# Performance work log

Hardware: AMD Instinct MI355X
Metric: run time of the kernel (lower is better)

## Reference

```python
import jax, jax.numpy as jnp
import numpy as np

B, MBITS, P = 4096, 64, 64
BLK = P // 8          # 8: block size for crop-robust pattern
FREQ = P // 4         # 16: low-res frequency pattern size
KS, SIGMA = 5, 1.0


def _interp_matrix(n_in, n_out):
    # 1D bilinear interpolation matrix with align_corners=True semantics
    pos = jnp.arange(n_out, dtype=jnp.float32) * (n_in - 1) / (n_out - 1)
    lo = jnp.floor(pos).astype(jnp.int32)
    hi = jnp.minimum(lo + 1, n_in - 1)
    w = pos - lo.astype(jnp.float32)
    rows = jnp.arange(n_out)
    M = jnp.zeros((n_out, n_in), jnp.float32)
    M = M.at[rows, lo].add(1.0 - w).at[rows, hi].add(w)
    return M


def _gaussian_kernel(ks, sigma):
    c = jnp.arange(ks, dtype=jnp.float32) - ks // 2
    g = jnp.exp(-c**2 / (2.0 * sigma**2))
    g = g / g.sum()
    k2 = jnp.outer(g, g)
    return k2 / k2.sum()


def setup_inputs() -> dict:
    key = jax.random.key(0)
    ks = jax.random.split(key, 8)

    def lin(k, fan_in, fan_out):
        lim = 1.0 / np.sqrt(fan_in)
        return jax.random.uniform(k, (fan_in, fan_out), jnp.float32, -lim, lim)

    return {
        'message': jax.random.uniform(ks[0], (B, MBITS), jnp.float32),
        'sW1': lin(ks[1], MBITS, 256), 'sb1': jnp.zeros((256,), jnp.float32),
        'sW2': lin(ks[2], 256, 512),   'sb2': jnp.zeros((512,), jnp.float32),
        'sW3': lin(ks[3], 512, P * P), 'sb3': jnp.zeros((P * P,), jnp.float32),
        'fW1': lin(ks[4], MBITS, 128), 'fb1': jnp.zeros((128,), jnp.float32),
        'fW2': lin(ks[5], 128, FREQ * FREQ), 'fb2': jnp.zeros((FREQ * FREQ,), jnp.float32),
    }


def reference(message, sW1, sb1, sW2, sb2, sW3, sb3, fW1, fb1, fW2, fb2):
    b = message.shape[0]
    # --- spatial pattern: MLP -> tanh -> [B,1,P,P]
    h = jax.nn.relu(message @ sW1 + sb1)
    h = jax.nn.relu(h @ sW2 + sb2)
    spatial = jnp.tanh(h @ sW3 + sb3).reshape(b, 1, P, P)

    # --- frequency pattern: MLP -> tanh -> [B,1,16,16] -> bilinear upsample to PxP
    f = jax.nn.relu(message @ fW1 + fb1)
    freq_lo = jnp.tanh(f @ fW2 + fb2).reshape(b, FREQ, FREQ)
    M = _interp_matrix(FREQ, P)  # [P, FREQ]
    freq = jnp.einsum('ph,bhw,qw->bpq', M, freq_lo, M)[:, None]  # [B,1,P,P]

    # --- block pattern: bit i -> 8x8 block (row-major over an 8x8 grid)
    blocks = message.reshape(b, 8, 8)  # [B, rows, cols] of bits
    block = jnp.repeat(jnp.repeat(blocks, BLK, axis=1), BLK, axis=2)[:, None]  # [B,1,P,P]

    rgb = jnp.concatenate([spatial, freq, block], axis=1)  # [B,3,P,P]

    # --- depthwise 5x5 Gaussian smoothing, groups=3
    k2 = _gaussian_kernel(KS, SIGMA)
    kernel = jnp.broadcast_to(k2, (3, 1, KS, KS))
    out = jax.lax.conv_general_dilated(
        rgb, kernel, window_strides=(1, 1), padding=[(KS // 2, KS // 2)] * 2,
        dimension_numbers=('NCHW', 'OIHW', 'NCHW'), feature_group_count=3)
    return out
```

## Files before the change

kernel.cpp:

```cpp
#include <hip/hip_runtime.h>
#include <math.h>

#define BATCH 4096

typedef __attribute__((ext_vector_type(8))) short short8;
typedef __attribute__((ext_vector_type(4))) float f32x4;

__device__ __forceinline__ unsigned short f2bf(float f) {
  unsigned int u = __float_as_uint(f);
  u += 0x7FFF + ((u >> 16) & 1);
  return (unsigned short)(u >> 16);
}

__device__ __forceinline__ float bf2f(unsigned short s) {
  return __uint_as_float(((unsigned int)s) << 16);
}

__device__ __forceinline__ float fast_tanh(float x) {
  const float e = __expf(2.0f * x);
  const float r = __builtin_amdgcn_rcpf(e + 1.0f);
  return fmaf(-2.0f, r, 1.0f);
}

#define GLL16(g, l)                                                    \
  __builtin_amdgcn_global_load_lds(                                    \
      (const __attribute__((address_space(1))) unsigned int*)(g),      \
      (__attribute__((address_space(3))) unsigned int*)(l), 16, 0, 0)

__global__ __launch_bounds__(256) void prep_kernel(
    const float* __restrict__ sW1, const float* __restrict__ sW2,
    const float* __restrict__ sW3, const float* __restrict__ msg,
    unsigned short* __restrict__ w1T, unsigned short* __restrict__ w2T,
    unsigned short* __restrict__ w3T, unsigned short* __restrict__ msgb) {
  const int b = blockIdx.x;
  const int t = threadIdx.x;

  if (b >= 2192) {
    const int i0 = (b - 2192) * 2048 + t * 8;
    const float4 v0 = *reinterpret_cast<const float4*>(&msg[i0]);
    const float4 v1 = *reinterpret_cast<const float4*>(&msg[i0 + 4]);
    short8 o;
    o[0] = (short)f2bf(v0.x); o[1] = (short)f2bf(v0.y);
    o[2] = (short)f2bf(v0.z); o[3] = (short)f2bf(v0.w);
    o[4] = (short)f2bf(v1.x); o[5] = (short)f2bf(v1.y);
    o[6] = (short)f2bf(v1.z); o[7] = (short)f2bf(v1.w);
    *reinterpret_cast<short8*>(&msgb[i0]) = o;
    return;
  }

  const float* src;
  unsigned short* dst;
  int K, N, lgtN, tile;
  if (b < 16) {
    src = sW1; dst = w1T; K = 64; N = 256; lgtN = 3; tile = b;
  } else if (b < 144) {
    src = sW2; dst = w2T; K = 256; N = 512; lgtN = 4; tile = b - 16;
  } else {
    src = sW3; dst = w3T; K = 512; N = 4096; lgtN = 7; tile = b - 144;
  }
  const int ty = tile >> lgtN;
  const int tx = tile & ((1 << lgtN) - 1);

  __shared__ float tl[32][33];
  {
    const int r = t >> 3, c4 = (t & 7) * 4;
    const float4 v =
        *reinterpret_cast<const float4*>(&src[(size_t)(ty * 32 + r) * N + tx * 32 + c4]);
    tl[r][c4 + 0] = v.x; tl[r][c4 + 1] = v.y;
    tl[r][c4 + 2] = v.z; tl[r][c4 + 3] = v.w;
  }
  __syncthreads();
  {
    const int nl = t >> 3, k4 = (t & 7) * 4;
    unsigned short o[4];
#pragma unroll
    for (int i = 0; i < 4; ++i) o[i] = f2bf(tl[k4 + i][nl]);
    *reinterpret_cast<ushort4*>(&dst[(size_t)(tx * 32 + nl) * K + ty * 32 + k4]) =
        *reinterpret_cast<const ushort4*>(o);
  }
}

template <int ACT, int OBF16, int KDIM>
__global__ __launch_bounds__(256) void gemm_mfma(
    const unsigned short* __restrict__ A, const unsigned short* __restrict__ BT,
    const float* __restrict__ bias, void* __restrict__ Cv, int ldc) {
  __shared__ __align__(16) unsigned short As[128 * 32];
  __shared__ __align__(16) unsigned short Bs[128 * 32];

  const int t = threadIdx.x;
  const int lane = t & 63;
  const int w = t >> 6;
  const int bm = blockIdx.x * 128;
  const int bn = blockIdx.y * 128;

  const int r0 = w * 32 + (lane >> 2);
  const int r1 = r0 + 16;
  const int c0 = (lane & 3) ^ ((r0 >> 1) & 3);
  const int c1 = (lane & 3) ^ ((r1 >> 1) & 3);

  const unsigned short* gA0 = A + (size_t)(bm + r0) * KDIM + c0 * 8;
  const unsigned short* gA1 = A + (size_t)(bm + r1) * KDIM + c1 * 8;
  const unsigned short* gB0 = BT + (size_t)(bn + r0) * KDIM + c0 * 8;
  const unsigned short* gB1 = BT + (size_t)(bn + r1) * KDIM + c1 * 8;

  unsigned short* lA0 = &As[(w * 2 + 0) * 512];
  unsigned short* lA1 = &As[(w * 2 + 1) * 512];
  unsigned short* lB0 = &Bs[(w * 2 + 0) * 512];
  unsigned short* lB1 = &Bs[(w * 2 + 1) * 512];

  const int wm = (w >> 1) * 64;
  const int wn = (w & 1) * 64;
  const int lr = lane & 15;
  const int lc = lane >> 4;
  int aoff[4], boff[4];
#pragma unroll
  for (int i = 0; i < 4; ++i) {
    const int row = wm + i * 16 + lr;
    aoff[i] = row * 32 + (lc ^ ((row >> 1) & 3)) * 8;
    const int col = wn + i * 16 + lr;
    boff[i] = col * 32 + (lc ^ ((col >> 1) & 3)) * 8;
  }

  f32x4 acc[4][4];
  const f32x4 z = {0.f, 0.f, 0.f, 0.f};
#pragma unroll
  for (int i = 0; i < 4; ++i)
#pragma unroll
    for (int j = 0; j < 4; ++j) acc[i][j] = z;

#pragma unroll 1
  for (int kt = 0; kt < KDIM / 32; ++kt) {
    GLL16(gA0, lA0);
    GLL16(gA1, lA1);
    GLL16(gB0, lB0);
    GLL16(gB1, lB1);
    __syncthreads();

    short8 a[4], b[4];
#pragma unroll
    for (int i = 0; i < 4; ++i) a[i] = *reinterpret_cast<const short8*>(&As[aoff[i]]);
#pragma unroll
    for (int j = 0; j < 4; ++j) b[j] = *reinterpret_cast<const short8*>(&Bs[boff[j]]);

#pragma unroll
    for (int i = 0; i < 4; ++i)
#pragma unroll
      for (int j = 0; j < 4; ++j)
        acc[i][j] =
            __builtin_amdgcn_mfma_f32_16x16x32_bf16(a[i], b[j], acc[i][j], 0, 0, 0);

    __syncthreads();
    gA0 += 32; gA1 += 32; gB0 += 32; gB1 += 32;
  }

  const int base_row = bm + wm + (lc << 2);
  const int base_col = bn + wn + lr;
#pragma unroll
  for (int i = 0; i < 4; ++i) {
#pragma unroll
    for (int j = 0; j < 4; ++j) {
      const int n = base_col + j * 16;
      const float bv = bias[n];
#pragma unroll
      for (int r = 0; r < 4; ++r) {
        const int m = base_row + i * 16 + r;
        float v = acc[i][j][r] + bv;
        v = (ACT == 0) ? fmaxf(v, 0.0f) : fast_tanh(v);
        if (OBF16)
          ((unsigned short*)Cv)[(size_t)m * ldc + n] = f2bf(v);
        else
          ((float*)Cv)[(size_t)m * ldc + n] = v;
      }
    }
  }
}

__global__ __launch_bounds__(256) void freq_mlp(
    const float* __restrict__ msg, const float* __restrict__ fW1,
    const float* __restrict__ fb1, const float* __restrict__ fW2,
    const float* __restrict__ fb2, float* __restrict__ fl) {
  const int row0 = blockIdx.x * 16;
  const int t = threadIdx.x;

  __shared__ float ms[16 * 64];
  __shared__ float f1[16][128];

  *reinterpret_cast<float4*>(&ms[t * 4]) =
      *reinterpret_cast<const float4*>(&msg[(size_t)row0 * 64 + t * 4]);
  __syncthreads();

  {
    const int n = t & 127;
    const int rb = (t >> 7) * 8;
    float acc[8] = {};
    for (int k = 0; k < 64; ++k) {
      const float wv = fW1[k * 128 + n];
#pragma unroll
      for (int r = 0; r < 8; ++r) acc[r] += ms[(rb + r) * 64 + k] * wv;
    }
    const float bv = fb1[n];
#pragma unroll
    for (int r = 0; r < 8; ++r) f1[rb + r][n] = fmaxf(acc[r] + bv, 0.0f);
  }
  __syncthreads();

  {
    float acc[16] = {};
    for (int k = 0; k < 128; ++k) {
      const float wv = fW2[k * 256 + t];
#pragma unroll
      for (int r = 0; r < 16; ++r) acc[r] += f1[r][k] * wv;
    }
    const float bv = fb2[t];
#pragma unroll
    for (int r = 0; r < 16; ++r)
      fl[(size_t)(row0 + r) * 256 + t] = fast_tanh(acc[r] + bv);
  }
}

__global__ __launch_bounds__(256) void finalize_kernel(
    const float* __restrict__ msg, const float* __restrict__ fl_in,
    const unsigned short* __restrict__ spatial, float* __restrict__ out) {
  const int b = blockIdx.x;
  const int c = blockIdx.y;
  const int t = threadIdx.x;

  __shared__ float chan[4096];
  __shared__ float tmp[4096];
  __shared__ float fl[256];
  __shared__ float msgs[64];
  __shared__ int lo_tab[64];
  __shared__ float w_tab[64];

  const float g0 = 0.054488684549644346f;
  const float g1 = 0.24420134200323332f;
  const float g2 = 0.4026199468907953f;
  const float g[5] = {g0, g1, g2, g1, g0};

  if (c != 0) {
    if (t < 64) {
      msgs[t] = msg[(size_t)b * 64 + t];
      const float pos = (float)t * (15.0f / 63.0f);
      int lo = (int)floorf(pos);
      if (lo > 15) lo = 15;
      lo_tab[t] = lo;
      w_tab[t] = pos - (float)lo;
    }
    fl[t] = fl_in[(size_t)b * 256 + t];
  }
  __syncthreads();

  if (c == 0) {
    const short8* sp = reinterpret_cast<const short8*>(spatial + (size_t)b * 4096);
    for (int v = t; v < 512; v += 256) {
      const short8 s = sp[v];
#pragma unroll
      for (int j = 0; j < 8; ++j) chan[v * 8 + j] = bf2f((unsigned short)s[j]);
    }
  } else if (c == 1) {
    for (int i = t; i < 4096; i += 256) {
      const int p = i >> 6, q = i & 63;
      const int lp = lo_tab[p], lq = lo_tab[q];
      const int hp = lp < 15 ? lp + 1 : 15;
      const int hq = lq < 15 ? lq + 1 : 15;
      const float wp = w_tab[p], wq = w_tab[q];
      const float v00 = fl[lp * 16 + lq], v01 = fl[lp * 16 + hq];
      const float v10 = fl[hp * 16 + lq], v11 = fl[hp * 16 + hq];
      chan[i] = (1.0f - wp) * ((1.0f - wq) * v00 + wq * v01) +
                wp * ((1.0f - wq) * v10 + wq * v11);
    }
  } else {
    for (int i = t; i < 4096; i += 256) {
      const int p = i >> 6, q = i & 63;
      chan[i] = msgs[((p >> 3) << 3) + (q >> 3)];
    }
  }
  __syncthreads();

  for (int i = t; i < 4096; i += 256) {
    const int p = i >> 6, q = i & 63;
    float s = 0.0f;
#pragma unroll
    for (int d = -2; d <= 2; ++d) {
      const int qq = q + d;
      if (qq >= 0 && qq < 64) s += g[d + 2] * chan[p * 64 + qq];
    }
    tmp[i] = s;
  }
  __syncthreads();

  float4* dst = reinterpret_cast<float4*>(out + (size_t)b * 12288 + (size_t)c * 4096);
  for (int i = t; i < 1024; i += 256) {
    const int p = i >> 4;
    const int q4 = (i & 15) * 4;
    float s0 = 0.f, s1 = 0.f, s2 = 0.f, s3 = 0.f;
#pragma unroll
    for (int d = -2; d <= 2; ++d) {
      const int pp = p + d;
      if (pp >= 0 && pp < 64) {
        const float gg = g[d + 2];
        const int base = pp * 64 + q4;
        s0 += gg * tmp[base + 0];
        s1 += gg * tmp[base + 1];
        s2 += gg * tmp[base + 2];
        s3 += gg * tmp[base + 3];
      }
    }
    float4 v;
    v.x = s0; v.y = s1; v.z = s2; v.w = s3;
    dst[i] = v;
  }
}

extern "C" void kernel_launch(void* const* d_in, const int* in_sizes, int n_in,
                              void* d_out, int out_size, void* d_ws,
                              size_t ws_size, hipStream_t stream) {
  const float* msg = (const float*)d_in[0];
  const float* sW1 = (const float*)d_in[1];
  const float* sb1 = (const float*)d_in[2];
  const float* sW2 = (const float*)d_in[3];
  const float* sb2 = (const float*)d_in[4];
  const float* sW3 = (const float*)d_in[5];
  const float* sb3 = (const float*)d_in[6];
  const float* fW1 = (const float*)d_in[7];
  const float* fb1 = (const float*)d_in[8];
  const float* fW2 = (const float*)d_in[9];
  const float* fb2 = (const float*)d_in[10];

  float* out = (float*)d_out;
  char* wsb = (char*)d_ws;

  unsigned short* msgb = (unsigned short*)(wsb);
  unsigned short* w1T  = (unsigned short*)(wsb + (1 << 19));
  unsigned short* w2T  = (unsigned short*)(wsb + (1 << 20));
  unsigned short* w3T  = (unsigned short*)(wsb + (2 << 20));
  unsigned short* h1   = (unsigned short*)(wsb + (8 << 20));
  unsigned short* h2   = (unsigned short*)(wsb + (12 << 20));
  unsigned short* spat = (unsigned short*)(wsb + (16 << 20));
  float* fl            = (float*)(wsb + (48 << 20));

  const dim3 blk(256);

  prep_kernel<<<dim3(2320), blk, 0, stream>>>(sW1, sW2, sW3, msg, w1T, w2T, w3T, msgb);

  gemm_mfma<0, 1, 64><<<dim3(32, 2), blk, 0, stream>>>(msgb, w1T, sb1, h1, 256);
  gemm_mfma<0, 1, 256><<<dim3(32, 4), blk, 0, stream>>>(h1, w2T, sb2, h2, 512);
  gemm_mfma<1, 1, 512><<<dim3(32, 32), blk, 0, stream>>>(h2, w3T, sb3, spat, 4096);

  freq_mlp<<<dim3(256), blk, 0, stream>>>(msg, fW1, fb1, fW2, fb2, fl);

  finalize_kernel<<<dim3(BATCH, 3), blk, 0, stream>>>(msg, fl, spat, out);
}
```

Before: 345.2 us.

## Merge freq MLP into prep kernel, double-buffer GEMM LDS, swizzle block order

Folds the frequency-MLP kernel into the weight/message prep kernel so one launch does both. The MFMA GEMM now double-buffers its LDS tiles, prefetching the next K tile while the current one is consumed, which removes one barrier per iteration. Workgroup indices are also remapped in an XCD-style swizzle to group neighbouring tiles. The cost is twice the LDS per block, which may lower occupancy, and the merged kernel's blocks now differ in their shared-memory use.

```diff
diff --git a/kernel.cpp b/kernel.cpp
--- a/kernel.cpp
+++ b/kernel.cpp
@@ -27,14 +27,56 @@
       (const __attribute__((address_space(1))) unsigned int*)(g),      \
       (__attribute__((address_space(3))) unsigned int*)(l), 16, 0, 0)
 
-__global__ __launch_bounds__(256) void prep_kernel(
+__global__ __launch_bounds__(256) void setup_kernel(
     const float* __restrict__ sW1, const float* __restrict__ sW2,
     const float* __restrict__ sW3, const float* __restrict__ msg,
+    const float* __restrict__ fW1, const float* __restrict__ fb1,
+    const float* __restrict__ fW2, const float* __restrict__ fb2,
     unsigned short* __restrict__ w1T, unsigned short* __restrict__ w2T,
-    unsigned short* __restrict__ w3T, unsigned short* __restrict__ msgb) {
-  const int b = blockIdx.x;
+    unsigned short* __restrict__ w3T, unsigned short* __restrict__ msgb,
+    float* __restrict__ fl) {
+  const int blk = blockIdx.x;
   const int t = threadIdx.x;
 
+  __shared__ float ms[16 * 64];
+  __shared__ float f1[16][128];
+  __shared__ float tl[32][33];
+
+  if (blk < 256) {
+    const int row0 = blk * 16;
+    *reinterpret_cast<float4*>(&ms[t * 4]) =
+        *reinterpret_cast<const float4*>(&msg[(size_t)row0 * 64 + t * 4]);
+    __syncthreads();
+    {
+      const int n = t & 127;
+      const int rb = (t >> 7) * 8;
+      float acc[8] = {};
+      for (int k = 0; k < 64; ++k) {
+        const float wv = fW1[k * 128 + n];
+#pragma unroll
+        for (int r = 0; r < 8; ++r) acc[r] += ms[(rb + r) * 64 + k] * wv;
+      }
+      const float bv = fb1[n];
+#pragma unroll
+      for (int r = 0; r < 8; ++r) f1[rb + r][n] = fmaxf(acc[r] + bv, 0.0f);
+    }
+    __syncthreads();
+    {
+      float acc[16] = {};
+      for (int k = 0; k < 128; ++k) {
+        const float wv = fW2[k * 256 + t];
+#pragma unroll
+        for (int r = 0; r < 16; ++r) acc[r] += f1[r][k] * wv;
+      }
+      const float bv = fb2[t];
+#pragma unroll
+      for (int r = 0; r < 16; ++r)
+        fl[(size_t)(row0 + r) * 256 + t] = fast_tanh(acc[r] + bv);
+    }
+    return;
+  }
+
+  const int b = blk - 256;
   if (b >= 2192) {
     const int i0 = (b - 2192) * 2048 + t * 8;
     const float4 v0 = *reinterpret_cast<const float4*>(&msg[i0]);
@@ -61,7 +103,6 @@
   const int ty = tile >> lgtN;
   const int tx = tile & ((1 << lgtN) - 1);
 
-  __shared__ float tl[32][33];
   {
     const int r = t >> 3, c4 = (t & 7) * 4;
     const float4 v =
@@ -80,18 +121,21 @@
   }
 }
 
-template <int ACT, int OBF16, int KDIM>
+template <int ACT, int OBF16, int KDIM, int NWG>
 __global__ __launch_bounds__(256) void gemm_mfma(
     const unsigned short* __restrict__ A, const unsigned short* __restrict__ BT,
     const float* __restrict__ bias, void* __restrict__ Cv, int ldc) {
-  __shared__ __align__(16) unsigned short As[128 * 32];
-  __shared__ __align__(16) unsigned short Bs[128 * 32];
+  __shared__ __align__(16) unsigned short As[2][128 * 32];
+  __shared__ __align__(16) unsigned short Bs[2][128 * 32];
 
   const int t = threadIdx.x;
   const int lane = t & 63;
   const int w = t >> 6;
-  const int bm = blockIdx.x * 128;
-  const int bn = blockIdx.y * 128;
+
+  const int orig = blockIdx.y * 32 + blockIdx.x;
+  const int swz = (orig & 7) * (NWG >> 3) + (orig >> 3);
+  const int bm = (swz & 31) * 128;
+  const int bn = (swz >> 5) * 128;
 
   const int r0 = w * 32 + (lane >> 2);
   const int r1 = r0 + 16;
@@ -103,10 +147,8 @@
   const unsigned short* gB0 = BT + (size_t)(bn + r0) * KDIM + c0 * 8;
   const unsigned short* gB1 = BT + (size_t)(bn + r1) * KDIM + c1 * 8;
 
-  unsigned short* lA0 = &As[(w * 2 + 0) * 512];
-  unsigned short* lA1 = &As[(w * 2 + 1) * 512];
-  unsigned short* lB0 = &Bs[(w * 2 + 0) * 512];
-  unsigned short* lB1 = &Bs[(w * 2 + 1) * 512];
+  const int lofs0 = (w * 2 + 0) * 512;
+  const int lofs1 = (w * 2 + 1) * 512;
 
   const int wm = (w >> 1) * 64;
   const int wn = (w & 1) * 64;
@@ -115,10 +157,10 @@
   int aoff[4], boff[4];
 #pragma unroll
   for (int i = 0; i < 4; ++i) {
-    const int row = wm + i * 16 + lr;
-    aoff[i] = row * 32 + (lc ^ ((row >> 1) & 3)) * 8;
-    const int col = wn + i * 16 + lr;
-    boff[i] = col * 32 + (lc ^ ((col >> 1) & 3)) * 8;
+    const int arow = wm + i * 16 + lr;
+    aoff[i] = arow * 32 + (lc ^ ((arow >> 1) & 3)) * 8;
+    const int brow = wn + i * 16 + lr;
+    boff[i] = brow * 32 + (lc ^ ((brow >> 1) & 3)) * 8;
   }
 
   f32x4 acc[4][4];
@@ -128,19 +170,34 @@
 #pragma unroll
     for (int j = 0; j < 4; ++j) acc[i][j] = z;
 
+  constexpr int NT = KDIM / 32;
+
+  GLL16(gA0, &As[0][lofs0]);
+  GLL16(gA1, &As[0][lofs1]);
+  GLL16(gB0, &Bs[0][lofs0]);
+  GLL16(gB1, &Bs[0][lofs1]);
+  gA0 += 32; gA1 += 32; gB0 += 32; gB1 += 32;
+  __syncthreads();
+
+  int cur = 0;
 #pragma unroll 1
-  for (int kt = 0; kt < KDIM / 32; ++kt) {
-    GLL16(gA0, lA0);
-    GLL16(gA1, lA1);
-    GLL16(gB0, lB0);
-    GLL16(gB1, lB1);
-    __syncthreads();
+  for (int kt = 0; kt < NT; ++kt) {
+    if (kt + 1 < NT) {
+      const int nxt = cur ^ 1;
+      GLL16(gA0, &As[nxt][lofs0]);
+      GLL16(gA1, &As[nxt][lofs1]);
+      GLL16(gB0, &Bs[nxt][lofs0]);
+      GLL16(gB1, &Bs[nxt][lofs1]);
+      gA0 += 32; gA1 += 32; gB0 += 32; gB1 += 32;
+    }
 
     short8 a[4], b[4];
 #pragma unroll
-    for (int i = 0; i < 4; ++i) a[i] = *reinterpret_cast<const short8*>(&As[aoff[i]]);
-#pragma unroll
-    for (int j = 0; j < 4; ++j) b[j] = *reinterpret_cast<const short8*>(&Bs[boff[j]]);
+    for (int i = 0; i < 4; ++i)
+      a[i] = *reinterpret_cast<const short8*>(&As[cur][aoff[i]]);
+#pragma unroll
+    for (int j = 0; j < 4; ++j)
+      b[j] = *reinterpret_cast<const short8*>(&Bs[cur][boff[j]]);
 
 #pragma unroll
     for (int i = 0; i < 4; ++i)
@@ -150,7 +207,7 @@
             __builtin_amdgcn_mfma_f32_16x16x32_bf16(a[i], b[j], acc[i][j], 0, 0, 0);
 
     __syncthreads();
-    gA0 += 32; gA1 += 32; gB0 += 32; gB1 += 32;
+    cur ^= 1;
   }
 
   const int base_row = bm + wm + (lc << 2);
@@ -172,49 +229,6 @@
           ((float*)Cv)[(size_t)m * ldc + n] = v;
       }
     }
-  }
-}
-
-__global__ __launch_bounds__(256) void freq_mlp(
-    const float* __restrict__ msg, const float* __restrict__ fW1,
-    const float* __restrict__ fb1, const float* __restrict__ fW2,
-    const float* __restrict__ fb2, float* __restrict__ fl) {
-  const int row0 = blockIdx.x * 16;
-  const int t = threadIdx.x;
-
-  __shared__ float ms[16 * 64];
-  __shared__ float f1[16][128];
-
-  *reinterpret_cast<float4*>(&ms[t * 4]) =
-      *reinterpret_cast<const float4*>(&msg[(size_t)row0 * 64 + t * 4]);
-  __syncthreads();
-
-  {
-    const int n = t & 127;
-    const int rb = (t >> 7) * 8;
-    float acc[8] = {};
-    for (int k = 0; k < 64; ++k) {
-      const float wv = fW1[k * 128 + n];
-#pragma unroll
-      for (int r = 0; r < 8; ++r) acc[r] += ms[(rb + r) * 64 + k] * wv;
-    }
-    const float bv = fb1[n];
-#pragma unroll
-    for (int r = 0; r < 8; ++r) f1[rb + r][n] = fmaxf(acc[r] + bv, 0.0f);
-  }
-  __syncthreads();
-
-  {
-    float acc[16] = {};
-    for (int k = 0; k < 128; ++k) {
-      const float wv = fW2[k * 256 + t];
-#pragma unroll
-      for (int r = 0; r < 16; ++r) acc[r] += f1[r][k] * wv;
-    }
-    const float bv = fb2[t];
-#pragma unroll
-    for (int r = 0; r < 16; ++r)
-      fl[(size_t)(row0 + r) * 256 + t] = fast_tanh(acc[r] + bv);
   }
 }
 
@@ -341,13 +355,12 @@
 
   const dim3 blk(256);
 
-  prep_kernel<<<dim3(2320), blk, 0, stream>>>(sW1, sW2, sW3, msg, w1T, w2T, w3T, msgb);
-
-  gemm_mfma<0, 1, 64><<<dim3(32, 2), blk, 0, stream>>>(msgb, w1T, sb1, h1, 256);
-  gemm_mfma<0, 1, 256><<<dim3(32, 4), blk, 0, stream>>>(h1, w2T, sb2, h2, 512);
-  gemm_mfma<1, 1, 512><<<dim3(32, 32), blk, 0, stream>>>(h2, w3T, sb3, spat, 4096);
-
-  freq_mlp<<<dim3(256), blk, 0, stream>>>(msg, fW1, fb1, fW2, fb2, fl);
+  setup_kernel<<<dim3(2576), blk, 0, stream>>>(sW1, sW2, sW3, msg, fW1, fb1,
+                                               fW2, fb2, w1T, w2T, w3T, msgb, fl);
+
+  gemm_mfma<0, 1, 64, 64><<<dim3(32, 2), blk, 0, stream>>>(msgb, w1T, sb1, h1, 256);
+  gemm_mfma<0, 1, 256, 128><<<dim3(32, 4), blk, 0, stream>>>(h1, w2T, sb2, h2, 512);
+  gemm_mfma<1, 1, 512, 1024><<<dim3(32, 32), blk, 0, stream>>>(h2, w3T, sb3, spat, 4096);
 
   finalize_kernel<<<dim3(BATCH, 3), blk, 0, stream>>>(msg, fl, spat, out);
 }
```

Measured after the change: 337.9 us. 2.1% less time.
